# Kernel optimization log

Hardware: AMD Instinct MI355X
Metric: run time of the kernel (lower is better)

Reference implementation:

```python
import jax, jax.numpy as jnp
import numpy as np

B, N, ND, H = 8, 1024, 64, 128
NUM_OPS, NUM_PARAMS, SKETCH = 64, 256, 128


def setup_inputs() -> dict:
    key = jax.random.key(0)
    ks = iter(jax.random.split(key, 64))

    def rn(shape, s=0.05):
        return jax.random.normal(next(ks), shape, dtype=jnp.float32) * s

    inp = {
        'node_features': jax.random.normal(next(ks), (B, N, ND), dtype=jnp.float32),
        'adjacency': (jax.random.uniform(next(ks), (B, N, N)) < 0.05).astype(jnp.float32),
        'mask': jnp.ones((B, N), jnp.float32),
    }
    for name, din in (('g1', ND), ('g2', H), ('g3', H)):
        inp[name + '_W'] = rn((din, H))
        inp[name + '_b'] = jnp.zeros((H,), jnp.float32)
        inp[name + '_aW'] = rn((2 * H,))
        inp[name + '_ab'] = jnp.zeros((), jnp.float32)
    for l in (0, 1):
        inp[f'l{l}_Wih'] = rn((4 * H, H))
        inp[f'l{l}_Whh'] = rn((4 * H, H))
        inp[f'l{l}_bih'] = jnp.zeros((4 * H,), jnp.float32)
        inp[f'l{l}_bhh'] = jnp.zeros((4 * H,), jnp.float32)
    for name, dout in (('op', NUM_OPS), ('pa', NUM_PARAMS), ('sk', SKETCH), ('no', ND)):
        inp[name + '_W1'] = rn((H, H))
        inp[name + '_b1'] = jnp.zeros((H,), jnp.float32)
        inp[name + '_W2'] = rn((H, dout))
        inp[name + '_b2'] = jnp.zeros((dout,), jnp.float32)
    return inp


def _gnn(x, adj, W, b, aW, ab):
    # h = Linear(x); att[b,i,j] = sigmoid(aW . [h_j ; h_i] + ab)  (cat order from the torch code)
    h = x @ W + b                      # [B,N,H]
    D = W.shape[1]
    sj = h @ aW[:D]                    # contribution of the dim-1-expanded term (h_j)
    si = h @ aW[D:]                    # contribution of the dim-2-expanded term (h_i)
    att = jax.nn.sigmoid(si[:, :, None] + sj[:, None, :] + ab) * adj  # [B,N,N]
    return jnp.einsum('bij,bjd->bid', att, h)


def _lstm(x, Wih, Whh, bih, bhh):
    # single torch-style LSTM layer, gate order i,f,g,o; zero initial state
    Bx, Hh = x.shape[0], Whh.shape[1]

    def step(carry, xt):
        h, c = carry
        g = xt @ Wih.T + h @ Whh.T + (bih + bhh)       # [B,4H]
        i, f, gg, o = jnp.split(g, 4, axis=-1)
        c = jax.nn.sigmoid(f) * c + jax.nn.sigmoid(i) * jnp.tanh(gg)
        h = jax.nn.sigmoid(o) * jnp.tanh(c)
        return (h, c), h

    z = jnp.zeros((Bx, Hh), x.dtype)
    _, ys = jax.lax.scan(step, (z, z), jnp.swapaxes(x, 0, 1))
    return jnp.swapaxes(ys, 0, 1)


def _mlp(x, W1, b1, W2, b2):
    return jax.nn.relu(x @ W1 + b1) @ W2 + b2


def reference(node_features, adjacency, mask,
              g1_W, g1_b, g1_aW, g1_ab,
              g2_W, g2_b, g2_aW, g2_ab,
              g3_W, g3_b, g3_aW, g3_ab,
              l0_Wih, l0_Whh, l0_bih, l0_bhh,
              l1_Wih, l1_Whh, l1_bih, l1_bhh,
              op_W1, op_b1, op_W2, op_b2,
              pa_W1, pa_b1, pa_W2, pa_b2,
              sk_W1, sk_b1, sk_W2, sk_b2,
              no_W1, no_b1, no_W2, no_b2):
    h = jax.nn.relu(_gnn(node_features, adjacency, g1_W, g1_b, g1_aW, g1_ab))
    h = jax.nn.relu(_gnn(h, adjacency, g2_W, g2_b, g2_aW, g2_ab))
    h = _gnn(h, adjacency, g3_W, g3_b, g3_aW, g3_ab)
    lo = _lstm(h, l0_Wih, l0_Whh, l0_bih, l0_bhh)
    lo = _lstm(lo, l1_Wih, l1_Whh, l1_bih, l1_bhh)
    op_pred = _mlp(lo, op_W1, op_b1, op_W2, op_b2)
    param_pred = _mlp(lo, pa_W1, pa_b1, pa_W2, pa_b2)
    sketch_pred = _mlp(lo, sk_W1, sk_b1, sk_W2, sk_b2)
    node_pred = _mlp(h, no_W1, no_b1, no_W2, no_b2)
    return (op_pred, param_pred, sketch_pred, node_pred)
```

## Files before the change

kernel.cpp:

```cpp
#include <hip/hip_runtime.h>

typedef __attribute__((ext_vector_type(8))) short short8;
typedef __attribute__((ext_vector_type(4))) float f32x4;
typedef __attribute__((ext_vector_type(2))) float f32x2;
typedef __attribute__((ext_vector_type(4))) unsigned short us4;
typedef __attribute__((ext_vector_type(2))) unsigned int u32x2;

__device__ __forceinline__ unsigned short bf16_of(float f) {
    unsigned u = __builtin_bit_cast(unsigned, f);
    u += 0x7fffu + ((u >> 16) & 1u);
    return (unsigned short)(u >> 16);
}
__device__ __forceinline__ unsigned bf16pk(float a, float b) {
    return (unsigned)bf16_of(a) | ((unsigned)bf16_of(b) << 16);
}
__device__ __forceinline__ float fexp2(float x) { return __builtin_amdgcn_exp2f(x); }
__device__ __forceinline__ float frcp(float x) { return __builtin_amdgcn_rcpf(x); }
__device__ __forceinline__ float sigm(float x) { return frcp(1.f + fexp2(-1.44269504f * x)); }
__device__ __forceinline__ float tanh_f(float x) {
    float e = fexp2(2.88539008f * x);
    return 1.f - 2.f * frcp(e + 1.f);
}
__device__ __forceinline__ f32x4 mfma16(short8 a, short8 b, f32x4 c) {
    return __builtin_amdgcn_mfma_f32_16x16x32_bf16(a, b, c, 0, 0, 0);
}
__device__ __forceinline__ float dpp_shr8(float x) {
    return __builtin_bit_cast(float, __builtin_amdgcn_update_dpp(
        0, __builtin_bit_cast(int, x), 0x118, 0xF, 0xF, true));
}
__device__ __forceinline__ float dpp_shl8(float x) {
    return __builtin_bit_cast(float, __builtin_amdgcn_update_dpp(
        0, __builtin_bit_cast(int, x), 0x108, 0xF, 0xF, true));
}

__global__ __launch_bounds__(256) void gemm_f32(
    const float* __restrict__ A, const float* __restrict__ B,
    const float* __restrict__ bias, float* __restrict__ C,
    int M, int N, int K, int BT, int RELU, int PACK)
{
    __shared__ float As[64][33];
    __shared__ float Bs[32][68];
    const int tid = threadIdx.x;
    const int tx = tid & 15, ty = tid >> 4;
    const int m0 = blockIdx.y * 64, n0 = blockIdx.x * 64;
    float acc[4][4];
#pragma unroll
    for (int i = 0; i < 4; ++i)
#pragma unroll
        for (int j = 0; j < 4; ++j) acc[i][j] = 0.f;

    for (int k0 = 0; k0 < K; k0 += 32) {
        __syncthreads();
        {
            const int r = tid >> 2, kk = (tid & 3) * 8;
            const float* src = A + (size_t)(m0 + r) * K + k0 + kk;
            f32x4 v0 = *(const f32x4*)src;
            f32x4 v1 = *(const f32x4*)(src + 4);
#pragma unroll
            for (int e = 0; e < 4; ++e) { As[r][kk + e] = v0[e]; As[r][kk + 4 + e] = v1[e]; }
        }
        if (!BT) {
            const int kk = tid >> 3, nn = (tid & 7) * 8;
            const float* src = B + (size_t)(k0 + kk) * N + n0 + nn;
            f32x4 v0 = *(const f32x4*)src;
            f32x4 v1 = *(const f32x4*)(src + 4);
#pragma unroll
            for (int e = 0; e < 4; ++e) { Bs[kk][nn + e] = v0[e]; Bs[kk][nn + 4 + e] = v1[e]; }
        } else {
            const int n = tid >> 2, kk = (tid & 3) * 8;
            const float* src = B + (size_t)(n0 + n) * K + k0 + kk;
            f32x4 v0 = *(const f32x4*)src;
            f32x4 v1 = *(const f32x4*)(src + 4);
#pragma unroll
            for (int e = 0; e < 4; ++e) { Bs[kk + e][n] = v0[e]; Bs[kk + 4 + e][n] = v1[e]; }
        }
        __syncthreads();
#pragma unroll 8
        for (int k = 0; k < 32; ++k) {
            float a0 = As[ty * 4 + 0][k], a1 = As[ty * 4 + 1][k];
            float a2 = As[ty * 4 + 2][k], a3 = As[ty * 4 + 3][k];
            f32x4 bv = *(const f32x4*)&Bs[k][tx * 4];
#pragma unroll
            for (int j = 0; j < 4; ++j) {
                acc[0][j] += a0 * bv[j]; acc[1][j] += a1 * bv[j];
                acc[2][j] += a2 * bv[j]; acc[3][j] += a3 * bv[j];
            }
        }
    }
    f32x4 bv = {};
    if (bias != nullptr) bv = *(const f32x4*)&bias[n0 + tx * 4];
#pragma unroll
    for (int i = 0; i < 4; ++i) {
        f32x4 res = {};
#pragma unroll
        for (int j = 0; j < 4; ++j) {
            float v = acc[i][j] + bv[j];
            if (RELU) v = fmaxf(v, 0.f);
            res[j] = v;
        }
        const int m = m0 + ty * 4 + i;
        if (!PACK) {
            *(f32x4*)&C[(size_t)m * N + n0 + tx * 4] = res;
        } else {
            const int b = m >> 10, t = m & 1023;
            const int n = n0 + tx * 4;
            const int pr = n >> 7, h = n & 127;
            *(f32x4*)&C[(((size_t)t * 4 + pr) * 8 + b) * 128 + h] = res;
        }
    }
}

__global__ __launch_bounds__(256) void sisj_kernel(
    const float* __restrict__ h, const float* __restrict__ aW,
    float* __restrict__ si, float* __restrict__ sj)
{
    const int tid = threadIdx.x, lane = tid & 63, w = tid >> 6;
    const int row = blockIdx.x * 4 + w;
    f32x2 hv = *(const f32x2*)(h + (size_t)row * 128 + lane * 2);
    f32x2 w1 = *(const f32x2*)&aW[lane * 2];
    f32x2 w2 = *(const f32x2*)&aW[128 + lane * 2];
    float sjp = hv[0] * w1[0] + hv[1] * w1[1];
    float sip = hv[0] * w2[0] + hv[1] * w2[1];
#pragma unroll
    for (int o = 32; o > 0; o >>= 1) {
        sjp += __shfl_xor(sjp, o);
        sip += __shfl_xor(sip, o);
    }
    if (lane == 0) { si[row] = sip; sj[row] = sjp; }
}

__global__ __launch_bounds__(256) void transpose_bf16_k(
    const float* __restrict__ h, unsigned short* __restrict__ hT)
{
    __shared__ float t[64][65];
    const int b = blockIdx.z, jt = blockIdx.x, dt = blockIdx.y;
    const int tid = threadIdx.x;
    const int r = tid >> 4, c4 = (tid & 15) * 4;
#pragma unroll
    for (int rr = 0; rr < 4; ++rr) {
        const int j = rr * 16 + r;
        f32x4 v = *(const f32x4*)(h + ((size_t)b * 1024 + jt * 64 + j) * 128 + dt * 64 + c4);
#pragma unroll
        for (int e = 0; e < 4; ++e) t[j][c4 + e] = v[e];
    }
    __syncthreads();
#pragma unroll
    for (int rr = 0; rr < 4; ++rr) {
        const int d = rr * 16 + r;
        u32x2 o;
        o[0] = bf16pk(t[c4 + 0][d], t[c4 + 1][d]);
        o[1] = bf16pk(t[c4 + 2][d], t[c4 + 3][d]);
        *(u32x2*)(hT + ((size_t)b * 128 + dt * 64 + d) * 1024 + jt * 64 + c4) = o;
    }
}

__global__ __launch_bounds__(256) void gnn_agg(
    const float* __restrict__ adj, const unsigned short* __restrict__ hT,
    const float* __restrict__ si, const float* __restrict__ sj,
    const float* __restrict__ abp, float* __restrict__ out, int RELU)
{
    __shared__ __align__(16) unsigned short Alds[64 * 40];
    __shared__ __align__(16) unsigned short Blds[128 * 40];
    const int b = blockIdx.y, it = blockIdx.x;
    const int i0 = it * 64;
    const int tid = threadIdx.x, lane = tid & 63, w = tid >> 6;
    const int quad = lane >> 4, col = lane & 15;
    const float ab = abp[0];
    const float* adjb = adj + (size_t)b * 1024 * 1024;
    const unsigned short* hTb = hT + (size_t)b * 128 * 1024;
    const float* sjb = sj + b * 1024;

    f32x4 acc[8] = {};
    const int ar_ = tid >> 2, ash = (tid & 3) * 8;
    const int br_ = tid >> 1, bsh = (tid & 1) * 16;
    const float sii = si[b * 1024 + i0 + ar_] + ab;

    for (int j0 = 0; j0 < 1024; j0 += 32) {
        __syncthreads();
        {
            const float* ar = adjb + (size_t)(i0 + ar_) * 1024 + j0 + ash;
            f32x4 av0 = *(const f32x4*)ar;
            f32x4 av1 = *(const f32x4*)(ar + 4);
            float s[8];
#pragma unroll
            for (int e = 0; e < 4; ++e) {
                s[e]     = sigm(sii + sjb[j0 + ash + e])     * av0[e];
                s[4 + e] = sigm(sii + sjb[j0 + ash + 4 + e]) * av1[e];
            }
            u32x2 o0 = {bf16pk(s[0], s[1]), bf16pk(s[2], s[3])};
            u32x2 o1 = {bf16pk(s[4], s[5]), bf16pk(s[6], s[7])};
            unsigned short* al = Alds + ar_ * 40 + ash;
            *(u32x2*)&al[0] = o0;
            *(u32x2*)&al[4] = o1;
        }
        {
            const unsigned short* bsrc = hTb + (size_t)br_ * 1024 + j0 + bsh;
            unsigned short* bl = Blds + br_ * 40 + bsh;
            *(short8*)&bl[0] = *(const short8*)&bsrc[0];
            *(short8*)&bl[8] = *(const short8*)&bsrc[8];
        }
        __syncthreads();
        short8 af = *(const short8*)&Alds[(w * 16 + col) * 40 + quad * 8];
#pragma unroll
        for (int nt = 0; nt < 8; ++nt) {
            short8 bf = *(const short8*)&Blds[(nt * 16 + col) * 40 + quad * 8];
            acc[nt] = mfma16(af, bf, acc[nt]);
        }
    }
    const int ibase = i0 + w * 16 + quad * 4;
#pragma unroll
    for (int nt = 0; nt < 8; ++nt) {
        const int d = nt * 16 + col;
#pragma unroll
        for (int r = 0; r < 4; ++r) {
            float v = acc[nt][r];
            if (RELU) v = fmaxf(v, 0.f);
            out[((size_t)b * 1024 + ibase + r) * 128 + d] = v;
        }
    }
}

__global__ void bsum_k(const float* a, const float* b, float* o) {
    const int i = threadIdx.x;
    o[i] = a[i] + b[i];
}
__global__ void zero_flags_k(int* f) { f[0] = 0; f[1] = 0; f[2] = 0; }


__device__ __forceinline__ void lstm_epilogue(
    const f32x4 accs[4], f32x4 xv0, f32x4 xv1, float* cst, float* hv, bool lo)
{
    float t0[4], t1[4];
#pragma unroll
    for (int i = 0; i < 4; ++i) {
        float P0 = 0.5f * ((lo ? accs[0][i] : dpp_shr8(accs[1][i])) + xv0[i]);
        float P1r = (lo ? accs[2][i] : dpp_shr8(accs[3][i])) + xv1[i];
        float P1 = lo ? P1r : 0.5f * P1r;
        t0[i] = tanh_f(P0);
        t1[i] = tanh_f(P1);
    }
    float c2[4], og[4];
#pragma unroll
    for (int i = 0; i < 4; ++i) {
        float ig = 0.5f + 0.5f * t0[i];
        float fg = 0.5f + 0.5f * dpp_shl8(t0[i]);
        float gg = t1[i];
        og[i] = 0.5f + 0.5f * dpp_shl8(t1[i]);
        c2[i] = fg * cst[i] + ig * gg;
        cst[i] = c2[i];
    }
    float pc0 = lo ? c2[0] : dpp_shr8(c2[1]);
    float pc1 = lo ? c2[2] : dpp_shr8(c2[3]);
    float tc0 = tanh_f(pc0), tc1 = tanh_f(pc1);
    float th[4] = {tc0, dpp_shl8(tc0), tc1, dpp_shl8(tc1)};
#pragma unroll
    for (int i = 0; i < 4; ++i) hv[i] = og[i] * th[i];
}

template <int OUT32>
__device__ __forceinline__ void lstm_step(
    unsigned short* Hc, unsigned short* Hn, const short8 afr[4][4],
    f32x4 xv0, f32x4 xv1, float* cst, void* __restrict__ sink,
    int t, int col, int quad, int h4, int b)
{
    short8 bfr[4];
#pragma unroll
    for (int c = 0; c < 4; ++c)
        bfr[c] = *(const short8*)&Hc[col * 136 + c * 32 + quad * 8];
    f32x4 accs[4] = {};
#pragma unroll
    for (int c = 0; c < 4; ++c)
#pragma unroll
        for (int g = 0; g < 4; ++g)
            accs[g] = mfma16(afr[g][c], bfr[c], accs[g]);

    const bool lo = (col < 8);
    float hv[4];
    lstm_epilogue(accs, xv0, xv1, cst, hv, lo);
    if (lo) {
        u32x2 hb = {bf16pk(hv[0], hv[1]), bf16pk(hv[2], hv[3])};
        *(u32x2*)&Hn[b * 136 + h4] = hb;
        if (OUT32) {
            f32x4 res = {hv[0], hv[1], hv[2], hv[3]};
            *(f32x4*)((float*)sink + ((size_t)b * 1024 + t) * 128 + h4) = res;
        } else {
            *(u32x2*)((unsigned short*)sink + (size_t)t * 1024 + b * 128 + h4) = hb;
        }
    }
    __builtin_amdgcn_s_waitcnt(0xC07F);
    __builtin_amdgcn_s_barrier();
}

__global__ __launch_bounds__(512) void lstm_pipe(
    const float* __restrict__ xw0, const float* __restrict__ Whh0,
    const float* __restrict__ Wih1, const float* __restrict__ Whh1,
    const float* __restrict__ bih1, const float* __restrict__ bhh1,
    unsigned short* __restrict__ hbuf, float* __restrict__ xw1,
    int* __restrict__ flags, float* __restrict__ out1)
{
    __shared__ __align__(16) unsigned short H[2][16 * 136];
    const int tid = threadIdx.x;
    const int lane = tid & 63;
    const int w = tid >> 6;
    const int quad = lane >> 4;
    const int col = lane & 15;
    const int b = col & 7;
    const int prA = col >> 3;
    const int h4 = w * 16 + quad * 4;

    if (blockIdx.x == 1) {
        short8 afrI[4][4];
        f32x4 biasv[4];
#pragma unroll
        for (int g = 0; g < 4; ++g) {
            const int row = g * 128 + w * 16 + col;
#pragma unroll
            for (int c = 0; c < 4; ++c) {
                const float* src = Wih1 + row * 128 + c * 32 + quad * 8;
                short8 v;
#pragma unroll
                for (int j = 0; j < 8; ++j) v[j] = (short)bf16_of(src[j]);
                afrI[g][c] = v;
            }
            const int rb = g * 128 + w * 16 + quad * 4;
            f32x4 b1 = *(const f32x4*)&bih1[rb];
            f32x4 b2 = *(const f32x4*)&bhh1[rb];
#pragma unroll
            for (int e = 0; e < 4; ++e) biasv[g][e] = b1[e] + b2[e];
        }
        for (int k = 0; k < 64; ++k) {
            while (__hip_atomic_load(&flags[0], __ATOMIC_ACQUIRE,
                                     __HIP_MEMORY_SCOPE_AGENT) < k + 1)
                __builtin_amdgcn_s_sleep(2);
            if (k >= 4) {
                while (__hip_atomic_load(&flags[2], __ATOMIC_RELAXED,
                                         __HIP_MEMORY_SCOPE_AGENT) < k - 3)
                    __builtin_amdgcn_s_sleep(2);
            }
            const unsigned short* hb = hbuf + (size_t)k * 16 * 1024;
            float* dst = xw1 + (size_t)(k & 3) * 65536;
#pragma unroll 2
            for (int nt = 0; nt < 8; ++nt) {
                const int tl = nt * 2 + (col >> 3);
                const unsigned short* src = hb + tl * 1024 + b * 128 + quad * 8;
                short8 bfr[4];
#pragma unroll
                for (int c = 0; c < 4; ++c) bfr[c] = *(const short8*)&src[c * 32];
                f32x4 acc[4] = {};
#pragma unroll
                for (int c = 0; c < 4; ++c)
#pragma unroll
                    for (int g = 0; g < 4; ++g)
                        acc[g] = mfma16(afrI[g][c], bfr[c], acc[g]);
#pragma unroll
                for (int g = 0; g < 4; ++g) {
                    f32x4 res;
#pragma unroll
                    for (int e = 0; e < 4; ++e) res[e] = acc[g][e] + biasv[g][e];
                    *(f32x4*)&dst[((tl * 4 + g) * 8 + b) * 128 + w * 16 + quad * 4] = res;
                }
            }
            __builtin_amdgcn_s_waitcnt(0x0F70);
            __builtin_amdgcn_s_barrier();
            if (tid == 0)
                __hip_atomic_store(&flags[1], k + 1, __ATOMIC_RELEASE,
                                   __HIP_MEMORY_SCOPE_AGENT);
        }
        return;
    }

    for (int i = tid; i < 2 * 16 * 136; i += 512) (&H[0][0])[i] = 0;
    float cst[4] = {0.f, 0.f, 0.f, 0.f};
    const int lane_off = (prA * 8 + b) * 128 + h4;

    if (blockIdx.x == 0) {
        short8 afr[4][4];
#pragma unroll
        for (int g = 0; g < 4; ++g) {
            const int row = g * 128 + w * 16 + col;
#pragma unroll
            for (int c = 0; c < 4; ++c) {
                const float* src = Whh0 + row * 128 + c * 32 + quad * 8;
                short8 v;
#pragma unroll
                for (int j = 0; j < 8; ++j) v[j] = (short)bf16_of(src[j]);
                afr[g][c] = v;
            }
        }
        const float* xp = xw0 + lane_off;
        f32x4 p0a = *(const f32x4*)(xp);
        f32x4 p1a = *(const f32x4*)(xp + 2048);
        f32x4 p0b = *(const f32x4*)(xp + 4096);
        f32x4 p1b = *(const f32x4*)(xp + 6144);
        xp += 8192;
        __syncthreads();

        for (int t = 0; t < 1024; t += 2) {
            const float* xr = (t == 1022) ? xp - 8192 : xp;
            {
                f32x4 xv0 = p0a, xv1 = p1a;
                p0a = *(const f32x4*)(xr);
                p1a = *(const f32x4*)(xr + 2048);
                lstm_step<0>(&H[0][0], &H[1][0], afr, xv0, xv1, cst, hbuf, t, col, quad, h4, b);
            }
            {
                f32x4 xv0 = p0b, xv1 = p1b;
                p0b = *(const f32x4*)(xr + 4096);
                p1b = *(const f32x4*)(xr + 6144);
                lstm_step<0>(&H[1][0], &H[0][0], afr, xv0, xv1, cst, hbuf, t + 1, col, quad, h4, b);
            }
            xp += 8192;
            if ((t & 14) == 14) {
                __syncthreads();
                if (tid == 0)
                    __hip_atomic_store(&flags[0], (t >> 4) + 1, __ATOMIC_RELEASE,
                                       __HIP_MEMORY_SCOPE_AGENT);
            }
        }
    } else {
        short8 afr[4][4];
#pragma unroll
        for (int g = 0; g < 4; ++g) {
            const int row = g * 128 + w * 16 + col;
#pragma unroll
            for (int c = 0; c < 4; ++c) {
                const float* src = Whh1 + row * 128 + c * 32 + quad * 8;
                short8 v;
#pragma unroll
                for (int j = 0; j < 8; ++j) v[j] = (short)bf16_of(src[j]);
                afr[g][c] = v;
            }
        }
        __syncthreads();
        auto xaddr = [&](int t) -> const float* {
            return xw1 + (((t >> 4) & 3) * 65536 + (t & 15) * 4096) + lane_off;
        };
        while (__hip_atomic_load(&flags[1], __ATOMIC_ACQUIRE,
                                 __HIP_MEMORY_SCOPE_AGENT) < 2)
            __builtin_amdgcn_s_sleep(2);
        f32x4 p0a = *(const f32x4*)xaddr(0);
        f32x4 p1a = *(const f32x4*)(xaddr(0) + 2048);
        f32x4 p0b = *(const f32x4*)xaddr(1);
        f32x4 p1b = *(const f32x4*)(xaddr(1) + 2048);

        for (int c = 0; c < 64; ++c) {
            if (c > 0) {
                const int target = (c + 2 < 64) ? c + 2 : 64;
                while (__hip_atomic_load(&flags[1], __ATOMIC_ACQUIRE,
                                         __HIP_MEMORY_SCOPE_AGENT) < target)
                    __builtin_amdgcn_s_sleep(2);
            }
            for (int s = 0; s < 16; s += 2) {
                const int t = c * 16 + s;
                const int t2 = (t + 2 < 1024) ? t + 2 : 1023;
                const int t3 = (t + 3 < 1024) ? t + 3 : 1023;
                {
                    f32x4 xv0 = p0a, xv1 = p1a;
                    p0a = *(const f32x4*)xaddr(t2);
                    p1a = *(const f32x4*)(xaddr(t2) + 2048);
                    lstm_step<1>(&H[0][0], &H[1][0], afr, xv0, xv1, cst, out1, t, col, quad, h4, b);
                }
                {
                    f32x4 xv0 = p0b, xv1 = p1b;
                    p0b = *(const f32x4*)xaddr(t3);
                    p1b = *(const f32x4*)(xaddr(t3) + 2048);
                    lstm_step<1>(&H[1][0], &H[0][0], afr, xv0, xv1, cst, out1, t + 1, col, quad, h4, b);
                }
            }
            if (tid == 0)
                __hip_atomic_store(&flags[2], c + 1, __ATOMIC_RELAXED,
                                   __HIP_MEMORY_SCOPE_AGENT);
        }
    }
}

extern "C" void kernel_launch(void* const* d_in, const int* in_sizes, int n_in,
                              void* d_out, int out_size, void* d_ws, size_t ws_size,
                              hipStream_t stream)
{
    (void)in_sizes; (void)n_in; (void)out_size; (void)ws_size;
    const float* nf    = (const float*)d_in[0];
    const float* adj   = (const float*)d_in[1];
    const float* g1W   = (const float*)d_in[3];
    const float* g1b   = (const float*)d_in[4];
    const float* g1aW  = (const float*)d_in[5];
    const float* g1ab  = (const float*)d_in[6];
    const float* g2W   = (const float*)d_in[7];
    const float* g2b   = (const float*)d_in[8];
    const float* g2aW  = (const float*)d_in[9];
    const float* g2ab  = (const float*)d_in[10];
    const float* g3W   = (const float*)d_in[11];
    const float* g3b   = (const float*)d_in[12];
    const float* g3aW  = (const float*)d_in[13];
    const float* g3ab  = (const float*)d_in[14];
    const float* l0Wih = (const float*)d_in[15];
    const float* l0Whh = (const float*)d_in[16];
    const float* l0bih = (const float*)d_in[17];
    const float* l0bhh = (const float*)d_in[18];
    const float* l1Wih = (const float*)d_in[19];
    const float* l1Whh = (const float*)d_in[20];
    const float* l1bih = (const float*)d_in[21];
    const float* l1bhh = (const float*)d_in[22];
    const float* opW1 = (const float*)d_in[23];
    const float* opb1 = (const float*)d_in[24];
    const float* opW2 = (const float*)d_in[25];
    const float* opb2 = (const float*)d_in[26];
    const float* paW1 = (const float*)d_in[27];
    const float* pab1 = (const float*)d_in[28];
    const float* paW2 = (const float*)d_in[29];
    const float* pab2 = (const float*)d_in[30];
    const float* skW1 = (const float*)d_in[31];
    const float* skb1 = (const float*)d_in[32];
    const float* skW2 = (const float*)d_in[33];
    const float* skb2 = (const float*)d_in[34];
    const float* noW1 = (const float*)d_in[35];
    const float* nob1 = (const float*)d_in[36];
    const float* noW2 = (const float*)d_in[37];
    const float* nob2 = (const float*)d_in[38];

    float* out = (float*)d_out;
    float* ws = (float*)d_ws;
    float* bufH  = ws;
    float* bufX  = ws + 1048576;
    float* bufH3 = ws + 2097152;
    unsigned short* bufT = (unsigned short*)(ws + 3145728);
    float* siB  = ws + 3670016;
    float* sjB  = ws + 3678208;
    float* bsum = ws + 3686400;
    float* out1 = ws + 3687424;
    float* xw0  = ws + 4736000;
    float* xw1  = ws + 8930304;
    int*  flags = (int*)(ws + 9192448);
    unsigned short* hbuf = (unsigned short*)bufX;

    auto gemm = [&](const float* A, const float* B, const float* bias, float* C,
                    int M, int N, int K, int BT, int RELU, int PACK = 0) {
        dim3 g(N / 64, M / 64);
        gemm_f32<<<g, dim3(256), 0, stream>>>(A, B, bias, C, M, N, K, BT, RELU, PACK);
    };

    gemm(nf, g1W, g1b, bufH, 8192, 128, 64, 0, 0);
    sisj_kernel<<<2048, 256, 0, stream>>>(bufH, g1aW, siB, sjB);
    transpose_bf16_k<<<dim3(16, 2, 8), 256, 0, stream>>>(bufH, bufT);
    gnn_agg<<<dim3(16, 8), 256, 0, stream>>>(adj, bufT, siB, sjB, g1ab, bufX, 1);
    gemm(bufX, g2W, g2b, bufH, 8192, 128, 128, 0, 0);
    sisj_kernel<<<2048, 256, 0, stream>>>(bufH, g2aW, siB, sjB);
    transpose_bf16_k<<<dim3(16, 2, 8), 256, 0, stream>>>(bufH, bufT);
    gnn_agg<<<dim3(16, 8), 256, 0, stream>>>(adj, bufT, siB, sjB, g2ab, bufX, 1);
    gemm(bufX, g3W, g3b, bufH, 8192, 128, 128, 0, 0);
    sisj_kernel<<<2048, 256, 0, stream>>>(bufH, g3aW, siB, sjB);
    transpose_bf16_k<<<dim3(16, 2, 8), 256, 0, stream>>>(bufH, bufT);
    gnn_agg<<<dim3(16, 8), 256, 0, stream>>>(adj, bufT, siB, sjB, g3ab, bufH3, 0);

    bsum_k<<<1, 512, 0, stream>>>(l0bih, l0bhh, bsum);
    gemm(bufH3, l0Wih, bsum, xw0, 8192, 512, 128, 1, 0, 1);
    zero_flags_k<<<1, 1, 0, stream>>>(flags);
    lstm_pipe<<<3, 512, 0, stream>>>(xw0, l0Whh, l1Wih, l1Whh, l1bih, l1bhh,
                                     hbuf, xw1, flags, out1);

    gemm(out1, opW1, opb1, bufH, 8192, 128, 128, 0, 1);
    gemm(bufH, opW2, opb2, out + 0, 8192, 64, 128, 0, 0);
    gemm(out1, paW1, pab1, bufH, 8192, 128, 128, 0, 1);
    gemm(bufH, paW2, pab2, out + 524288, 8192, 256, 128, 0, 0);
    gemm(out1, skW1, skb1, bufH, 8192, 128, 128, 0, 1);
    gemm(bufH, skW2, skb2, out + 2621440, 8192, 128, 128, 0, 0);
    gemm(bufH3, noW1, nob1, bufH, 8192, 128, 128, 0, 1);
    gemm(bufH, noW2, nob2, out + 3670016, 8192, 64, 128, 0, 0);
}
```

Measured before the change: 1.427 ms.

## Fuse MLP heads into LSTM pipeline kernel, overlapping them with recurrence

Adds 8 extra blocks to the persistent LSTM kernel. They compute the node head right away and the op/param/sketch heads on each 128-row strip once the layer-1 LSTM signals that the chunk is done. This replaces eight separate GEMM launches that ran after the recurrence. A prep kernel pre-transposes the head weights to bf16 and also does the bias-sum and flag-zeroing, and the LSTM output is now stored as bf16. Spin-waits are limited to one thread followed by a barrier. Risks include extra contention from the co-running blocks, bf16 rounding of the LSTM output, and correctness of the flag ordering.

New measurement: 1.401 ms. About the same (-1.8%).

```diff
diff --git a/kernel.cpp b/kernel.cpp
--- a/kernel.cpp
+++ b/kernel.cpp
@@ -220,12 +220,46 @@
     }
 }
 
-__global__ void bsum_k(const float* a, const float* b, float* o) {
-    const int i = threadIdx.x;
-    o[i] = a[i] + b[i];
-}
-__global__ void zero_flags_k(int* f) { f[0] = 0; f[1] = 0; f[2] = 0; }
-
+struct PrepArgs {
+    const float* src[8];
+    unsigned short* dst[8];
+    int N[8];
+};
+__global__ __launch_bounds__(256) void prep_k(
+    PrepArgs pa, const float* bih0, const float* bhh0,
+    float* bsum, int* flags)
+{
+    const int m = blockIdx.x;
+    const int tid = threadIdx.x;
+    if (m < 8) {
+        const float* src = pa.src[m];
+        unsigned short* dst = pa.dst[m];
+        const int N = pa.N[m];
+        const int n0 = tid >> 4, kc = (tid & 15) * 8;
+        for (int n = n0; n < N; n += 16) {
+            unsigned o[4];
+#pragma unroll
+            for (int e = 0; e < 8; e += 2)
+                o[e >> 1] = bf16pk(src[(size_t)(kc + e) * N + n],
+                                   src[(size_t)(kc + e + 1) * N + n]);
+            *(u32x2*)&dst[n * 128 + kc] = *(u32x2*)&o[0];
+            *(u32x2*)&dst[n * 128 + kc + 4] = *(u32x2*)&o[2];
+        }
+    } else {
+        bsum[tid] = bih0[tid] + bhh0[tid];
+        bsum[tid + 256] = bih0[tid + 256] + bhh0[tid + 256];
+        if (tid < 3) flags[tid] = 0;
+    }
+}
+
+
+struct HeadArgs {
+    const unsigned short* W1T[4];
+    const float* b1[4];
+    const unsigned short* W2T[4];
+    const float* b2[4];
+    float* outp[4];
+};
 
 __device__ __forceinline__ void lstm_epilogue(
     const f32x4 accs[4], f32x4 xv0, f32x4 xv1, float* cst, float* hv, bool lo)
@@ -257,10 +291,10 @@
     for (int i = 0; i < 4; ++i) hv[i] = og[i] * th[i];
 }
 
-template <int OUT32>
+template <int SINK>
 __device__ __forceinline__ void lstm_step(
     unsigned short* Hc, unsigned short* Hn, const short8 afr[4][4],
-    f32x4 xv0, f32x4 xv1, float* cst, void* __restrict__ sink,
+    f32x4 xv0, f32x4 xv1, float* cst, unsigned short* __restrict__ sink,
     int t, int col, int quad, int h4, int b)
 {
     short8 bfr[4];
@@ -280,15 +314,86 @@
     if (lo) {
         u32x2 hb = {bf16pk(hv[0], hv[1]), bf16pk(hv[2], hv[3])};
         *(u32x2*)&Hn[b * 136 + h4] = hb;
-        if (OUT32) {
-            f32x4 res = {hv[0], hv[1], hv[2], hv[3]};
-            *(f32x4*)((float*)sink + ((size_t)b * 1024 + t) * 128 + h4) = res;
-        } else {
-            *(u32x2*)((unsigned short*)sink + (size_t)t * 1024 + b * 128 + h4) = hb;
-        }
+        if (SINK == 0)
+            *(u32x2*)(sink + (size_t)t * 1024 + b * 128 + h4) = hb;
+        else
+            *(u32x2*)(sink + ((size_t)t * 8 + b) * 128 + h4) = hb;
     }
     __builtin_amdgcn_s_waitcnt(0xC07F);
     __builtin_amdgcn_s_barrier();
+}
+
+template <int A32, int LROWS>
+__device__ void head_strip(
+    const void* __restrict__ Asrc, int row0,
+    const unsigned short* __restrict__ W1T, const float* __restrict__ b1,
+    const unsigned short* __restrict__ W2T, const float* __restrict__ b2,
+    float* __restrict__ outp, int dout, unsigned short* A2, int tid)
+{
+    const int lane = tid & 63, w = tid >> 6;
+    const int quad = lane >> 4, col = lane & 15;
+    const int mrow = w * 16 + col;
+    f32x4 acc[8] = {};
+#pragma unroll
+    for (int kc = 0; kc < 4; ++kc) {
+        short8 af;
+        if (A32) {
+            const float* s = (const float*)Asrc + (size_t)(row0 + mrow) * 128 + kc * 32 + quad * 8;
+            f32x4 v0 = *(const f32x4*)s, v1 = *(const f32x4*)(s + 4);
+            short8 v;
+#pragma unroll
+            for (int j = 0; j < 4; ++j) {
+                v[j] = (short)bf16_of(v0[j]);
+                v[4 + j] = (short)bf16_of(v1[j]);
+            }
+            af = v;
+        } else {
+            af = *(const short8*)((const unsigned short*)Asrc +
+                                  (size_t)(row0 + mrow) * 128 + kc * 32 + quad * 8);
+        }
+#pragma unroll
+        for (int nt = 0; nt < 8; ++nt) {
+            short8 bf = *(const short8*)&W1T[(nt * 16 + col) * 128 + kc * 32 + quad * 8];
+            acc[nt] = mfma16(af, bf, acc[nt]);
+        }
+    }
+    float b1v[8];
+#pragma unroll
+    for (int nt = 0; nt < 8; ++nt) b1v[nt] = b1[nt * 16 + col];
+    __syncthreads();
+#pragma unroll
+    for (int nt = 0; nt < 8; ++nt)
+#pragma unroll
+        for (int i = 0; i < 4; ++i) {
+            const int mm = w * 16 + quad * 4 + i;
+            A2[mm * 136 + nt * 16 + col] = bf16_of(fmaxf(acc[nt][i] + b1v[nt], 0.f));
+        }
+    __syncthreads();
+    const int ntiles = dout >> 4;
+    for (int np = 0; np < ntiles; np += 8) {
+        const int nts = (ntiles - np < 8) ? ntiles - np : 8;
+        f32x4 acc2[8] = {};
+#pragma unroll
+        for (int kc = 0; kc < 4; ++kc) {
+            short8 a2f = *(const short8*)&A2[mrow * 136 + kc * 32 + quad * 8];
+            for (int nt = 0; nt < nts; ++nt) {
+                short8 bf = *(const short8*)&W2T[((np + nt) * 16 + col) * 128 + kc * 32 + quad * 8];
+                acc2[nt] = mfma16(a2f, bf, acc2[nt]);
+            }
+        }
+        for (int nt = 0; nt < nts; ++nt) {
+            const int n = (np + nt) * 16 + col;
+            const float bb = b2[n];
+#pragma unroll
+            for (int i = 0; i < 4; ++i) {
+                const int r = row0 + w * 16 + quad * 4 + i;
+                size_t off;
+                if (LROWS) off = ((size_t)(r & 7) * 1024 + (r >> 3)) * dout + n;
+                else       off = (size_t)r * dout + n;
+                outp[off] = acc2[nt][i] + bb;
+            }
+        }
+    }
 }
 
 __global__ __launch_bounds__(512) void lstm_pipe(
@@ -296,9 +401,11 @@
     const float* __restrict__ Wih1, const float* __restrict__ Whh1,
     const float* __restrict__ bih1, const float* __restrict__ bhh1,
     unsigned short* __restrict__ hbuf, float* __restrict__ xw1,
-    int* __restrict__ flags, float* __restrict__ out1)
+    int* __restrict__ flags, unsigned short* __restrict__ out1b,
+    const float* __restrict__ bufH3, HeadArgs ha)
 {
     __shared__ __align__(16) unsigned short H[2][16 * 136];
+    __shared__ __align__(16) unsigned short A2[128 * 136];
     const int tid = threadIdx.x;
     const int lane = tid & 63;
     const int w = tid >> 6;
@@ -308,6 +415,28 @@
     const int prA = col >> 3;
     const int h4 = w * 16 + quad * 4;
 
+    if (blockIdx.x >= 3) {
+        const int wid = blockIdx.x - 3;
+        for (int s = wid; s < 64; s += 8)
+            head_strip<1, 0>(bufH3, s * 128, ha.W1T[3], ha.b1[3],
+                             ha.W2T[3], ha.b2[3], ha.outp[3], 64, A2, tid);
+        for (int s = wid; s < 64; s += 8) {
+            if (tid == 0) {
+                while (__hip_atomic_load(&flags[2], __ATOMIC_ACQUIRE,
+                                         __HIP_MEMORY_SCOPE_AGENT) < s + 1)
+                    __builtin_amdgcn_s_sleep(16);
+            }
+            __syncthreads();
+            head_strip<0, 1>(out1b, s * 128, ha.W1T[0], ha.b1[0],
+                             ha.W2T[0], ha.b2[0], ha.outp[0], 64, A2, tid);
+            head_strip<0, 1>(out1b, s * 128, ha.W1T[1], ha.b1[1],
+                             ha.W2T[1], ha.b2[1], ha.outp[1], 256, A2, tid);
+            head_strip<0, 1>(out1b, s * 128, ha.W1T[2], ha.b1[2],
+                             ha.W2T[2], ha.b2[2], ha.outp[2], 128, A2, tid);
+        }
+        return;
+    }
+
     if (blockIdx.x == 1) {
         short8 afrI[4][4];
         f32x4 biasv[4];
@@ -329,14 +458,18 @@
             for (int e = 0; e < 4; ++e) biasv[g][e] = b1[e] + b2[e];
         }
         for (int k = 0; k < 64; ++k) {
-            while (__hip_atomic_load(&flags[0], __ATOMIC_ACQUIRE,
-                                     __HIP_MEMORY_SCOPE_AGENT) < k + 1)
-                __builtin_amdgcn_s_sleep(2);
-            if (k >= 4) {
-                while (__hip_atomic_load(&flags[2], __ATOMIC_RELAXED,
-                                         __HIP_MEMORY_SCOPE_AGENT) < k - 3)
+            if (tid == 0) {
+                while (__hip_atomic_load(&flags[0], __ATOMIC_ACQUIRE,
+                                         __HIP_MEMORY_SCOPE_AGENT) < k + 1)
                     __builtin_amdgcn_s_sleep(2);
-            }
+                if (k >= 4) {
+                    while (__hip_atomic_load(&flags[2], __ATOMIC_RELAXED,
+                                             __HIP_MEMORY_SCOPE_AGENT) < k - 3)
+                        __builtin_amdgcn_s_sleep(2);
+                }
+            }
+            __builtin_amdgcn_s_waitcnt(0xC07F);
+            __builtin_amdgcn_s_barrier();
             const unsigned short* hb = hbuf + (size_t)k * 16 * 1024;
             float* dst = xw1 + (size_t)(k & 3) * 65536;
 #pragma unroll 2
@@ -446,9 +579,13 @@
         for (int c = 0; c < 64; ++c) {
             if (c > 0) {
                 const int target = (c + 2 < 64) ? c + 2 : 64;
-                while (__hip_atomic_load(&flags[1], __ATOMIC_ACQUIRE,
-                                         __HIP_MEMORY_SCOPE_AGENT) < target)
-                    __builtin_amdgcn_s_sleep(2);
+                if (tid == 0) {
+                    while (__hip_atomic_load(&flags[1], __ATOMIC_ACQUIRE,
+                                             __HIP_MEMORY_SCOPE_AGENT) < target)
+                        __builtin_amdgcn_s_sleep(2);
+                }
+                __builtin_amdgcn_s_waitcnt(0xC07F);
+                __builtin_amdgcn_s_barrier();
             }
             for (int s = 0; s < 16; s += 2) {
                 const int t = c * 16 + s;
@@ -458,17 +595,18 @@
                     f32x4 xv0 = p0a, xv1 = p1a;
                     p0a = *(const f32x4*)xaddr(t2);
                     p1a = *(const f32x4*)(xaddr(t2) + 2048);
-                    lstm_step<1>(&H[0][0], &H[1][0], afr, xv0, xv1, cst, out1, t, col, quad, h4, b);
+                    lstm_step<1>(&H[0][0], &H[1][0], afr, xv0, xv1, cst, out1b, t, col, quad, h4, b);
                 }
                 {
                     f32x4 xv0 = p0b, xv1 = p1b;
                     p0b = *(const f32x4*)xaddr(t3);
                     p1b = *(const f32x4*)(xaddr(t3) + 2048);
-                    lstm_step<1>(&H[1][0], &H[0][0], afr, xv0, xv1, cst, out1, t + 1, col, quad, h4, b);
+                    lstm_step<1>(&H[1][0], &H[0][0], afr, xv0, xv1, cst, out1b, t + 1, col, quad, h4, b);
                 }
             }
+            __syncthreads();
             if (tid == 0)
-                __hip_atomic_store(&flags[2], c + 1, __ATOMIC_RELAXED,
+                __hip_atomic_store(&flags[2], c + 1, __ATOMIC_RELEASE,
                                    __HIP_MEMORY_SCOPE_AGENT);
         }
     }
@@ -527,11 +665,21 @@
     float* siB  = ws + 3670016;
     float* sjB  = ws + 3678208;
     float* bsum = ws + 3686400;
-    float* out1 = ws + 3687424;
-    float* xw0  = ws + 4736000;
-    float* xw1  = ws + 8930304;
-    int*  flags = (int*)(ws + 9192448);
+    float* xw0  = ws + 3687424;
+    float* xw1  = ws + 7881728;
+    int*  flags = (int*)(ws + 8143872);
+    unsigned short* WT = (unsigned short*)(ws + 8143876);
+    unsigned short* out1b = (unsigned short*)(ws + 8209412);
     unsigned short* hbuf = (unsigned short*)bufX;
+
+    unsigned short* opW1T = WT;
+    unsigned short* paW1T = WT + 16384;
+    unsigned short* skW1T = WT + 32768;
+    unsigned short* noW1T = WT + 49152;
+    unsigned short* opW2T = WT + 65536;
+    unsigned short* paW2T = WT + 73728;
+    unsigned short* skW2T = WT + 106496;
+    unsigned short* noW2T = WT + 122880;
 
     auto gemm = [&](const float* A, const float* B, const float* bias, float* C,
                     int M, int N, int K, int BT, int RELU, int PACK = 0) {
@@ -552,18 +700,28 @@
     transpose_bf16_k<<<dim3(16, 2, 8), 256, 0, stream>>>(bufH, bufT);
     gnn_agg<<<dim3(16, 8), 256, 0, stream>>>(adj, bufT, siB, sjB, g3ab, bufH3, 0);
 
-    bsum_k<<<1, 512, 0, stream>>>(l0bih, l0bhh, bsum);
+    PrepArgs pargs;
+    pargs.src[0] = opW1; pargs.dst[0] = opW1T; pargs.N[0] = 128;
+    pargs.src[1] = paW1; pargs.dst[1] = paW1T; pargs.N[1] = 128;
+    pargs.src[2] = skW1; pargs.dst[2] = skW1T; pargs.N[2] = 128;
+    pargs.src[3] = noW1; pargs.dst[3] = noW1T; pargs.N[3] = 128;
+    pargs.src[4] = opW2; pargs.dst[4] = opW2T; pargs.N[4] = 64;
+    pargs.src[5] = paW2; pargs.dst[5] = paW2T; pargs.N[5] = 256;
+    pargs.src[6] = skW2; pargs.dst[6] = skW2T; pargs.N[6] = 128;
+    pargs.src[7] = noW2; pargs.dst[7] = noW2T; pargs.N[7] = 64;
+    prep_k<<<9, 256, 0, stream>>>(pargs, l0bih, l0bhh, bsum, flags);
+
     gemm(bufH3, l0Wih, bsum, xw0, 8192, 512, 128, 1, 0, 1);
-    zero_flags_k<<<1, 1, 0, stream>>>(flags);
-    lstm_pipe<<<3, 512, 0, stream>>>(xw0, l0Whh, l1Wih, l1Whh, l1bih, l1bhh,
-                                     hbuf, xw1, flags, out1);
-
-    gemm(out1, opW1, opb1, bufH, 8192, 128, 128, 0, 1);
-    gemm(bufH, opW2, opb2, out + 0, 8192, 64, 128, 0, 0);
-    gemm(out1, paW1, pab1, bufH, 8192, 128, 128, 0, 1);
-    gemm(bufH, paW2, pab2, out + 524288, 8192, 256, 128, 0, 0);
-    gemm(out1, skW1, skb1, bufH, 8192, 128, 128, 0, 1);
-    gemm(bufH, skW2, skb2, out + 2621440, 8192, 128, 128, 0, 0);
-    gemm(bufH3, noW1, nob1, bufH, 8192, 128, 128, 0, 1);
-    gemm(bufH, noW2, nob2, out + 3670016, 8192, 64, 128, 0, 0);
-}
+
+    HeadArgs ha;
+    ha.W1T[0] = opW1T; ha.b1[0] = opb1; ha.W2T[0] = opW2T; ha.b2[0] = opb2;
+    ha.outp[0] = out + 0;
+    ha.W1T[1] = paW1T; ha.b1[1] = pab1; ha.W2T[1] = paW2T; ha.b2[1] = pab2;
+    ha.outp[1] = out + 524288;
+    ha.W1T[2] = skW1T; ha.b1[2] = skb1; ha.W2T[2] = skW2T; ha.b2[2] = skb2;
+    ha.outp[2] = out + 2621440;
+    ha.W1T[3] = noW1T; ha.b1[3] = nob1; ha.W2T[3] = noW2T; ha.b2[3] = nob2;
+    ha.outp[3] = out + 3670016;
+    lstm_pipe<<<11, 512, 0, stream>>>(xw0, l0Whh, l1Wih, l1Whh, l1bih, l1bhh,
+                                      hbuf, xw1, flags, out1b, bufH3, ha);
+}
```
